# Kernel optimization log

Hardware: AMD Instinct MI355X
Metric: run time of the kernel (lower is better)

## Reference

```python
import jax, jax.numpy as jnp
import numpy as np

CHANNELS = 64
WEIGHT_NUMS = [66 * 64, 64 * 64, 64]  # layer0 (C+2)->C, layer1 C->C, layer2 C->1
BIAS_NUMS = [64, 64, 1]
NUM_GEN_PARAMS = sum(WEIGHT_NUMS) + sum(BIAS_NUMS)  # 8513


def setup_inputs() -> dict:
    key = jax.random.key(0)
    k1, k2 = jax.random.split(key)
    N, C, H, W = 4, 64, 80, 200
    num_ins = 8  # instances per image -> M = 32 total
    M = N * num_ins
    x = jax.random.normal(k1, (N, C, H, W), dtype=jnp.float32)
    mask_head_params = jax.random.normal(k2, (M, NUM_GEN_PARAMS), dtype=jnp.float32) * 0.1
    return {"x": x, "mask_head_params": mask_head_params, "num_ins": num_ins}


def reference(x, mask_head_params, num_ins):
    N, C, H, W = x.shape
    ch = CHANNELS
    # compute_locations with stride=1 (stride//2 == 0); source bug divides the
    # whole tensor by W (locations[:1,:,:] /= W on a batch-1 tensor).
    xx, yy = jnp.meshgrid(jnp.arange(W, dtype=x.dtype), jnp.arange(H, dtype=x.dtype), indexing='xy')
    loc = jnp.stack([xx, yy], axis=0) / W  # [2, H, W]
    xa = jnp.concatenate([jnp.broadcast_to(loc[None], (N, 2, H, W)), x], axis=1)  # [N, C+2, H, W]
    feats = jnp.repeat(xa, num_ins, axis=0)  # [M, C+2, H, W] per-instance inputs
    M = feats.shape[0]
    # parse_dynamic_params: split generated params into per-layer weights/biases
    splits = np.cumsum(WEIGHT_NUMS + BIAS_NUMS)[:-1]
    w0, w1, w2, b0, b1, b2 = jnp.split(mask_head_params, splits, axis=1)
    w0 = w0.reshape(M, ch, ch + 2)
    w1 = w1.reshape(M, ch, ch)
    w2 = w2.reshape(M, 1, ch)
    b2 = b2 - 2.19  # mask bias shift (is_mask=True)
    # grouped 1x1 convs (groups=M) as per-instance GEMMs with ReLU between layers
    h = jax.nn.relu(jnp.einsum('mkc,mchw->mkhw', w0, feats) + b0[:, :, None, None])
    h = jax.nn.relu(jnp.einsum('mkc,mchw->mkhw', w1, h) + b1[:, :, None, None])
    out = jnp.einsum('mkc,mchw->mkhw', w2, h) + b2[:, :, None, None]
    return out.reshape(1, -1, H, W)  # [1, M*out_channels, H, W]
```

## Files before the change

### kernel.cpp

```cpp
#include <hip/hip_runtime.h>

typedef __attribute__((ext_vector_type(8)))  short    short8;
typedef __attribute__((ext_vector_type(4)))  short    s16x4;
typedef __attribute__((ext_vector_type(4)))  float    f32x4;
typedef __attribute__((ext_vector_type(4)))  unsigned uint4_;
typedef __attribute__((ext_vector_type(2)))  unsigned uint2_;

#define HW     16000
#define WWID   200
#define NPARAM 8513
#define PACK_STRIDE 6144

__device__ __forceinline__ unsigned pkbf2(float a, float b) {
    unsigned r;
    asm("v_cvt_pk_bf16_f32 %0, %1, %2" : "=v"(r) : "v"(a), "v"(b));
    return r;
}
__device__ __forceinline__ short8 mk8(unsigned a, unsigned b, unsigned c, unsigned d) {
    uint4_ u; u.x = a; u.y = b; u.z = c; u.w = d;
    return __builtin_bit_cast(short8, u);
}
__device__ __forceinline__ s16x4 mk4(unsigned a, unsigned b) {
    uint2_ u; u.x = a; u.y = b;
    return __builtin_bit_cast(s16x4, u);
}
__device__ __forceinline__ void mfma16(f32x4& acc, s16x4 a, s16x4 b) {
    asm("s_nop 2\n\tv_mfma_f32_16x16x16_bf16 %0, %1, %2, %0"
        : "+v"(acc) : "v"(a), "v"(b));
}

__device__ __forceinline__ float w0val(const float* pm, int k, int c) {
    if (c < 64)  return pm[k * 66 + c + 2];
    if (c == 64) return pm[k * 66 + 0];
    if (c == 65) return pm[k * 66 + 1];
    if (c == 66) return pm[8384 + k];
    return 0.0f;
}

__global__ __launch_bounds__(256) void pack_weights(
    const float* __restrict__ params, unsigned* __restrict__ wp)
{
    const int m   = blockIdx.x;
    const int tid = threadIdx.x;
    const float* pm = params + (size_t)m * NPARAM;
    unsigned* dst = wp + (size_t)m * PACK_STRIDE;

    if (blockIdx.y == 0) {
        const int l  = tid >> 2;
        const int i0 = (tid & 3) * 2;
        #pragma unroll
        for (int frag = 0; frag < 12; ++frag) {
            int ch = frag >> 2, kb = frag & 3;
            int k = kb * 16 + (l & 15);
            int c = ch * 32 + (l >> 4) * 8 + i0;
            dst[frag * 256 + tid] = pkbf2(w0val(pm, k, c), w0val(pm, k, c + 1));
        }
        float* fd = (float*)dst;
        if (tid < 64) {
            fd[5120 + tid] = pm[8448 + tid];
            fd[5184 + tid] = pm[8320 + tid];
        }
        if (tid == 0) fd[5248] = pm[8512];
    } else {
        #pragma unroll
        for (int i = tid; i < 2048; i += 256) {
            int f = i >> 7, r = i & 127;
            int l = r >> 1, d = i & 1;
            int kb = f >> 2, ks = f & 3;
            int row = kb * 16 + (l & 15);
            int col = ks * 16 + (l >> 4) * 4 + d * 2;
            const float* s = pm + 4224 + row * 64 + col;
            dst[3072 + i] = pkbf2(s[0], s[1]);
        }
    }
}

__global__ __launch_bounds__(512, 3) void condlane_reg(
    const float* __restrict__ x,
    const unsigned* __restrict__ wp,
    float* __restrict__ out,
    int num_ins)
{
    extern __shared__ char lds_[];
    char* xt = lds_;
    const int tid  = threadIdx.x;
    const int lane = tid & 63;
    const int wid  = tid >> 6;
    const int n    = blockIdx.y;
    const int pxg0 = blockIdx.x * 256;
    const int g    = (lane >> 4) & 3;
    const int px16 = lane & 15;

    {
        const int p   = tid & 255;
        const int sel = tid >> 8;
        const int pc  = min(pxg0 + p, HW - 1);
        const float* xp = x + (size_t)n * 64 * HW + pc;
        #pragma unroll
        for (int it = 0; it < 4; ++it) {
            int c0 = sel * 32 + it * 8;
            uint4_ d;
            d.x = pkbf2(xp[(size_t)(c0 + 0) * HW], xp[(size_t)(c0 + 1) * HW]);
            d.y = pkbf2(xp[(size_t)(c0 + 2) * HW], xp[(size_t)(c0 + 3) * HW]);
            d.z = pkbf2(xp[(size_t)(c0 + 4) * HW], xp[(size_t)(c0 + 5) * HW]);
            d.w = pkbf2(xp[(size_t)(c0 + 6) * HW], xp[(size_t)(c0 + 7) * HW]);
            *(uint4_*)(xt + ((p * 256 + c0 * 2) ^ ((p & 15) << 4))) = d;
        }
        const int pg = pxg0 + p;
        float lx = (float)(pg % WWID) * (1.0f / WWID);
        float ly = (float)(pg / WWID) * (1.0f / WWID);
        uint4_ z;  z.x = 0; z.y = 0; z.z = 0; z.w = 0;
        uint4_ cv; cv.x = pkbf2(lx, ly); cv.y = pkbf2(1.f, 0.f); cv.z = 0; cv.w = 0;
        int ba = (p * 256 + 128 + sel * 32) ^ ((p & 15) << 4);
        int bb = (p * 256 + 144 + sel * 32) ^ ((p & 15) << 4);
        *(uint4_*)(xt + ba) = (sel == 0) ? cv : z;
        *(uint4_*)(xt + bb) = z;
    }

    const int m = n * num_ins + wid;
    const unsigned* wm = wp + (size_t)m * PACK_STRIDE;

    short8 w0f[3][4];
    s16x4  w1f4[4][4];
    #pragma unroll
    for (int ch = 0; ch < 3; ++ch)
        #pragma unroll
        for (int kb = 0; kb < 4; ++kb)
            w0f[ch][kb] = *(const short8*)(wm + (ch * 4 + kb) * 256 + lane * 4);
    #pragma unroll
    for (int kb = 0; kb < 4; ++kb)
        #pragma unroll
        for (int ks = 0; ks < 4; ++ks)
            w1f4[kb][ks] = *(const s16x4*)(wm + 3072 + (kb * 4 + ks) * 128 + lane * 2);
    const float* fm = (const float*)wm;
    f32x4 bias1[4], w2v[4];
    #pragma unroll
    for (int kb = 0; kb < 4; ++kb) {
        bias1[kb] = *(const f32x4*)(fm + 5120 + kb * 16 + g * 4);
        w2v[kb]   = *(const f32x4*)(fm + 5184 + kb * 16 + g * 4);
    }
    const float b2 = fm[5248] - 2.19f;

    __syncthreads();

    const int swz = px16 << 4;
    const int nsl = min(16, (HW - pxg0) >> 4);

    for (int s = 0; s < 16; ++s) {
        const int pxl = s * 16 + px16;
        short8 xf[3];
        #pragma unroll
        for (int ch = 0; ch < 3; ++ch)
            xf[ch] = *(const short8*)(xt + ((pxl * 256 + ch * 64 + g * 16) ^ swz));
        f32x4 acc0[4];
        #pragma unroll
        for (int kb = 0; kb < 4; ++kb)
            #pragma unroll
            for (int j = 0; j < 4; ++j) acc0[kb][j] = 0.f;
        #pragma unroll
        for (int ch = 0; ch < 3; ++ch)
            #pragma unroll
            for (int kb = 0; kb < 4; ++kb)
                acc0[kb] = __builtin_amdgcn_mfma_f32_16x16x32_bf16(w0f[ch][kb], xf[ch], acc0[kb], 0, 0, 0);
        s16x4 hf[4];
        #pragma unroll
        for (int ks = 0; ks < 4; ++ks)
            hf[ks] = mk4(pkbf2(fmaxf(acc0[ks][0], 0.f), fmaxf(acc0[ks][1], 0.f)),
                         pkbf2(fmaxf(acc0[ks][2], 0.f), fmaxf(acc0[ks][3], 0.f)));
        f32x4 acc1[4];
        #pragma unroll
        for (int kb = 0; kb < 4; ++kb) acc1[kb] = bias1[kb];
        #pragma unroll
        for (int ks = 0; ks < 4; ++ks)
            #pragma unroll
            for (int kb = 0; kb < 4; ++kb)
                mfma16(acc1[kb], w1f4[kb][ks], hf[ks]);
        asm("s_nop 7\n\ts_nop 7"
            : "+v"(acc1[0]), "+v"(acc1[1]), "+v"(acc1[2]), "+v"(acc1[3]));
        float v = 0.f;
        #pragma unroll
        for (int kb = 0; kb < 4; ++kb)
            #pragma unroll
            for (int r = 0; r < 4; ++r)
                v += w2v[kb][r] * fmaxf(acc1[kb][r], 0.f);
        v += __shfl_xor(v, 16);
        v += __shfl_xor(v, 32);
        if (lane < 16 && s < nsl)
            out[(size_t)m * HW + pxg0 + s * 16 + lane] = v + b2;
    }
}

extern "C" void kernel_launch(void* const* d_in, const int* in_sizes, int n_in,
                              void* d_out, int out_size, void* d_ws, size_t ws_size,
                              hipStream_t stream) {
    const float* x      = (const float*)d_in[0];
    const float* params = (const float*)d_in[1];
    float* out          = (float*)d_out;

    const int N = in_sizes[0] / (64 * HW);
    const int M = in_sizes[1] / NPARAM;
    const int num_ins = M / N;

    pack_weights<<<dim3(M, 2), 256, 0, stream>>>(params, (unsigned*)d_ws);

    dim3 grid((HW + 255) / 256, N);
    condlane_reg<<<grid, 512, 65536, stream>>>(x, (const unsigned*)d_ws, out, num_ins);
}
```

Baseline: 26.85 us.

## Compute final projection via MFMA and batch layer-1 MFMAs in one asm block

Replaces the per-lane FMA dot product and two cross-lane shuffles of the last 64->1 layer with four bf16 MFMAs. The w2 row is packed into an A fragment that is nonzero only in row 0. The sixteen layer-1 MFMAs move into a single inline asm block with one leading nop instead of a nop before each MFMA. The first layer-0 MFMA now starts from a zero constant, and launch bounds drop to 2 blocks per SM. This trades VALU and shuffle work for extra matrix ops, adds bf16 rounding of the layer-2 inputs and weights, and may lower occupancy.

After: 26.72 us. About the same (-0.5%).

```diff
diff --git a/kernel.cpp b/kernel.cpp
--- a/kernel.cpp
+++ b/kernel.cpp
@@ -16,17 +16,9 @@
     asm("v_cvt_pk_bf16_f32 %0, %1, %2" : "=v"(r) : "v"(a), "v"(b));
     return r;
 }
-__device__ __forceinline__ short8 mk8(unsigned a, unsigned b, unsigned c, unsigned d) {
-    uint4_ u; u.x = a; u.y = b; u.z = c; u.w = d;
-    return __builtin_bit_cast(short8, u);
-}
 __device__ __forceinline__ s16x4 mk4(unsigned a, unsigned b) {
     uint2_ u; u.x = a; u.y = b;
     return __builtin_bit_cast(s16x4, u);
-}
-__device__ __forceinline__ void mfma16(f32x4& acc, s16x4 a, s16x4 b) {
-    asm("s_nop 2\n\tv_mfma_f32_16x16x16_bf16 %0, %1, %2, %0"
-        : "+v"(acc) : "v"(a), "v"(b));
 }
 
 __device__ __forceinline__ float w0val(const float* pm, int k, int c) {
@@ -75,7 +67,7 @@
     }
 }
 
-__global__ __launch_bounds__(512, 3) void condlane_reg(
+__global__ __launch_bounds__(512, 2) void condlane_reg(
     const float* __restrict__ x,
     const unsigned* __restrict__ wp,
     float* __restrict__ out,
@@ -121,7 +113,7 @@
     const unsigned* wm = wp + (size_t)m * PACK_STRIDE;
 
     short8 w0f[3][4];
-    s16x4  w1f4[4][4];
+    s16x4  w1f[4][4];
     #pragma unroll
     for (int ch = 0; ch < 3; ++ch)
         #pragma unroll
@@ -131,13 +123,20 @@
     for (int kb = 0; kb < 4; ++kb)
         #pragma unroll
         for (int ks = 0; ks < 4; ++ks)
-            w1f4[kb][ks] = *(const s16x4*)(wm + 3072 + (kb * 4 + ks) * 128 + lane * 2);
+            w1f[kb][ks] = *(const s16x4*)(wm + 3072 + (kb * 4 + ks) * 128 + lane * 2);
     const float* fm = (const float*)wm;
-    f32x4 bias1[4], w2v[4];
+    f32x4 bias1[4];
+    s16x4 w2A[4];
     #pragma unroll
     for (int kb = 0; kb < 4; ++kb) {
         bias1[kb] = *(const f32x4*)(fm + 5120 + kb * 16 + g * 4);
-        w2v[kb]   = *(const f32x4*)(fm + 5184 + kb * 16 + g * 4);
+        unsigned lo = 0u, hi = 0u;
+        if (px16 == 0) {
+            const float* w2p = fm + 5184 + kb * 16 + g * 4;
+            lo = pkbf2(w2p[0], w2p[1]);
+            hi = pkbf2(w2p[2], w2p[3]);
+        }
+        w2A[kb] = mk4(lo, hi);
     }
     const float b2 = fm[5248] - 2.19f;
 
@@ -145,6 +144,7 @@
 
     const int swz = px16 << 4;
     const int nsl = min(16, (HW - pxg0) >> 4);
+    f32x4 zero4; zero4[0] = 0.f; zero4[1] = 0.f; zero4[2] = 0.f; zero4[3] = 0.f;
 
     for (int s = 0; s < 16; ++s) {
         const int pxl = s * 16 + px16;
@@ -155,10 +155,9 @@
         f32x4 acc0[4];
         #pragma unroll
         for (int kb = 0; kb < 4; ++kb)
-            #pragma unroll
-            for (int j = 0; j < 4; ++j) acc0[kb][j] = 0.f;
-        #pragma unroll
-        for (int ch = 0; ch < 3; ++ch)
+            acc0[kb] = __builtin_amdgcn_mfma_f32_16x16x32_bf16(w0f[0][kb], xf[0], zero4, 0, 0, 0);
+        #pragma unroll
+        for (int ch = 1; ch < 3; ++ch)
             #pragma unroll
             for (int kb = 0; kb < 4; ++kb)
                 acc0[kb] = __builtin_amdgcn_mfma_f32_16x16x32_bf16(w0f[ch][kb], xf[ch], acc0[kb], 0, 0, 0);
@@ -170,23 +169,48 @@
         f32x4 acc1[4];
         #pragma unroll
         for (int kb = 0; kb < 4; ++kb) acc1[kb] = bias1[kb];
-        #pragma unroll
-        for (int ks = 0; ks < 4; ++ks)
-            #pragma unroll
-            for (int kb = 0; kb < 4; ++kb)
-                mfma16(acc1[kb], w1f4[kb][ks], hf[ks]);
+        asm("s_nop 2\n\t"
+            "v_mfma_f32_16x16x16_bf16 %0, %4, %20, %0\n\t"
+            "v_mfma_f32_16x16x16_bf16 %1, %5, %20, %1\n\t"
+            "v_mfma_f32_16x16x16_bf16 %2, %6, %20, %2\n\t"
+            "v_mfma_f32_16x16x16_bf16 %3, %7, %20, %3\n\t"
+            "v_mfma_f32_16x16x16_bf16 %0, %8, %21, %0\n\t"
+            "v_mfma_f32_16x16x16_bf16 %1, %9, %21, %1\n\t"
+            "v_mfma_f32_16x16x16_bf16 %2, %10, %21, %2\n\t"
+            "v_mfma_f32_16x16x16_bf16 %3, %11, %21, %3\n\t"
+            "v_mfma_f32_16x16x16_bf16 %0, %12, %22, %0\n\t"
+            "v_mfma_f32_16x16x16_bf16 %1, %13, %22, %1\n\t"
+            "v_mfma_f32_16x16x16_bf16 %2, %14, %22, %2\n\t"
+            "v_mfma_f32_16x16x16_bf16 %3, %15, %22, %3\n\t"
+            "v_mfma_f32_16x16x16_bf16 %0, %16, %23, %0\n\t"
+            "v_mfma_f32_16x16x16_bf16 %1, %17, %23, %1\n\t"
+            "v_mfma_f32_16x16x16_bf16 %2, %18, %23, %2\n\t"
+            "v_mfma_f32_16x16x16_bf16 %3, %19, %23, %3"
+            : "+v"(acc1[0]), "+v"(acc1[1]), "+v"(acc1[2]), "+v"(acc1[3])
+            : "v"(w1f[0][0]), "v"(w1f[1][0]), "v"(w1f[2][0]), "v"(w1f[3][0]),
+              "v"(w1f[0][1]), "v"(w1f[1][1]), "v"(w1f[2][1]), "v"(w1f[3][1]),
+              "v"(w1f[0][2]), "v"(w1f[1][2]), "v"(w1f[2][2]), "v"(w1f[3][2]),
+              "v"(w1f[0][3]), "v"(w1f[1][3]), "v"(w1f[2][3]), "v"(w1f[3][3]),
+              "v"(hf[0]), "v"(hf[1]), "v"(hf[2]), "v"(hf[3]));
         asm("s_nop 7\n\ts_nop 7"
             : "+v"(acc1[0]), "+v"(acc1[1]), "+v"(acc1[2]), "+v"(acc1[3]));
-        float v = 0.f;
+        s16x4 hg[4];
         #pragma unroll
         for (int kb = 0; kb < 4; ++kb)
-            #pragma unroll
-            for (int r = 0; r < 4; ++r)
-                v += w2v[kb][r] * fmaxf(acc1[kb][r], 0.f);
-        v += __shfl_xor(v, 16);
-        v += __shfl_xor(v, 32);
+            hg[kb] = mk4(pkbf2(fmaxf(acc1[kb][0], 0.f), fmaxf(acc1[kb][1], 0.f)),
+                         pkbf2(fmaxf(acc1[kb][2], 0.f), fmaxf(acc1[kb][3], 0.f)));
+        f32x4 acc2 = zero4;
+        asm("s_nop 2\n\t"
+            "v_mfma_f32_16x16x16_bf16 %0, %1, %5, %0\n\t"
+            "v_mfma_f32_16x16x16_bf16 %0, %2, %6, %0\n\t"
+            "v_mfma_f32_16x16x16_bf16 %0, %3, %7, %0\n\t"
+            "v_mfma_f32_16x16x16_bf16 %0, %4, %8, %0"
+            : "+v"(acc2)
+            : "v"(w2A[0]), "v"(w2A[1]), "v"(w2A[2]), "v"(w2A[3]),
+              "v"(hg[0]), "v"(hg[1]), "v"(hg[2]), "v"(hg[3]));
+        asm("s_nop 7\n\ts_nop 7" : "+v"(acc2));
         if (lane < 16 && s < nsl)
-            out[(size_t)m * HW + pxg0 + s * 16 + lane] = v + b2;
+            out[(size_t)m * HW + pxg0 + s * 16 + lane] = acc2[0] + b2;
     }
 }
 
```
